# Performance work log

Hardware: AMD Instinct MI355X
Metric: run time of the kernel (lower is better)

The kernel has to match this reference:

```python
import jax, jax.numpy as jnp
import numpy as np

N, E = 50000, 800000
F_IN, F_OUT, H, F_EDGE = 256, 32, 8, 5
LEAKY_SLOPE = 0.2


def setup_inputs() -> dict:
    key = jax.random.key(0)
    ks = jax.random.split(key, 6)
    x = jax.random.normal(ks[0], (N, F_IN), dtype=jnp.float32)
    edge_index = jax.random.randint(ks[1], (2, E), 0, N, dtype=jnp.int64)
    edge_attr = jax.random.normal(ks[2], (E, F_EDGE), dtype=jnp.float32)
    degree_src = jax.random.randint(ks[3], (E,), 0, 64, dtype=jnp.int64)
    # Xavier-uniform params
    lim_W = float(np.sqrt(6.0 / (F_IN + F_OUT)))
    W = jax.random.uniform(ks[4], (H, F_IN, F_OUT), minval=-lim_W, maxval=lim_W, dtype=jnp.float32)
    A = 2 * F_OUT + F_EDGE
    lim_a = float(np.sqrt(6.0 / (H + A)))
    a = jax.random.uniform(ks[5], (H, A), minval=-lim_a, maxval=lim_a, dtype=jnp.float32)
    lim_e = float(np.sqrt(1.0 / F_EDGE))
    W_edge_w = jax.random.uniform(jax.random.fold_in(key, 7), (F_EDGE, F_EDGE), minval=-lim_e, maxval=lim_e, dtype=jnp.float32)
    return {"x": x, "edge_index": edge_index, "edge_attr": edge_attr,
            "degree_src": degree_src, "W": W, "a": a, "W_edge_w": W_edge_w}


def reference(x, edge_index, edge_attr, degree_src, W, a, W_edge_w):
    n = x.shape[0]
    h, f_out = W.shape[0], W.shape[2]
    src, dst = edge_index[0], edge_index[1]
    # per-head projection: (N, H, F_out)
    Wh = jnp.einsum('nf,hfo->nho', x, W)
    # split attention vector instead of materializing the concat
    a_src, a_dst, a_e = a[:, :f_out], a[:, f_out:2 * f_out], a[:, 2 * f_out:]
    ef = edge_attr @ W_edge_w.T                      # (E, F_edge)
    e = (jnp.einsum('eho,ho->eh', Wh[src], a_src)
         + jnp.einsum('eho,ho->eh', Wh[dst], a_dst)
         + ef @ a_e.T)                                # (E, H)
    e = jax.nn.leaky_relu(e, LEAKY_SLOPE)
    scale = 1.0 / jnp.sqrt(jnp.clip(degree_src.astype(jnp.float32), 1.0, None))
    e = e * scale[:, None]
    # segment softmax over src; torch scatter_reduce amax include_self=True with zeros init -> max includes 0
    e_max = jnp.maximum(jax.ops.segment_max(e, src, num_segments=n), 0.0)
    e_exp = jnp.exp(e - e_max[src])
    e_sum = jax.ops.segment_sum(e_exp, src, num_segments=n)
    alpha = e_exp / (e_sum[src] + 1e-16)             # (E, H)
    msg = Wh[dst] * alpha[:, :, None]                # (E, H, F_out)
    out = jax.ops.segment_sum(msg, src, num_segments=n)
    out = jax.nn.elu(out.reshape(n, h * f_out))
    return out, alpha
```

## Files before the change

kernel.cpp:

```cpp
#include <hip/hip_runtime.h>
#include <hip/hip_bf16.h>
#include <math.h>

#define NN 50000
#define NE 800000
#define FIN 256
#define FOUT 32
#define NH 8
#define FE 5
#define AROW 69
#define NROWS_PAD 50048
#define BSTRIDE 48
#define ASTRIDE 264

typedef float f32x4 __attribute__((ext_vector_type(4)));
typedef short bf16x8 __attribute__((ext_vector_type(8)));

static __device__ __forceinline__ unsigned short f2bf(float f) {
    unsigned u = __float_as_uint(f);
    unsigned r = (u + 0x7FFFu + ((u >> 16) & 1u)) >> 16;
    return (unsigned short)r;
}
static __device__ __forceinline__ float bf2f(unsigned short b) {
    return __uint_as_float(((unsigned)b) << 16);
}
static __device__ __forceinline__ short f2bf_fast(float f) {
    __hip_bfloat16 h = __float2bfloat16(f);
    return *reinterpret_cast<short*>(&h);
}

__global__ __launch_bounds__(256) void k_prepre(const float* __restrict__ W,
                                                const float* __restrict__ a,
                                                const float* __restrict__ Wew,
                                                const int* __restrict__ ei,
                                                float* __restrict__ C,
                                                unsigned short* __restrict__ Bh,
                                                unsigned short* __restrict__ Bsh,
                                                unsigned short* __restrict__ Bsl,
                                                int* __restrict__ counts,
                                                int* __restrict__ pos) {
    int b = blockIdx.x, t = threadIdx.x;
    int i = b * 256 + t;
    if (i < NE / 4) {
        int4 e4 = *(const int4*)&ei[i * 4];
        int4 pv;
        pv.x = atomicAdd(&counts[e4.x], 1);
        pv.y = atomicAdd(&counts[e4.y], 1);
        pv.z = atomicAdd(&counts[e4.z], 1);
        pv.w = atomicAdd(&counts[e4.w], 1);
        *(int4*)&pos[i * 4] = pv;
    }
    if (b < 256) {
        int c = b, k = t;
        int h = c >> 5, o = c & 31;
        Bh[c * 256 + k] = f2bf(W[(size_t)h * (FIN * FOUT) + (size_t)k * FOUT + o]);
    } else if (b == 256) {
        if (t < NH * FE) {
            int h = t / FE, k = t % FE;
            float s = 0.f;
            for (int j = 0; j < FE; ++j) s += a[h * AROW + 2 * FOUT + j] * Wew[j * FE + k];
            C[t] = s;
        }
        int k = t;
        for (int h = 0; h < NH; ++h) {
            float s1v = 0.f, s2v = 0.f;
            for (int o = 0; o < FOUT; ++o) {
                float wv = W[(size_t)h * (FIN * FOUT) + (size_t)k * FOUT + o];
                s1v += wv * a[h * AROW + o];
                s2v += wv * a[h * AROW + FOUT + o];
            }
            unsigned short h1 = f2bf(s1v);
            Bsh[h * 256 + k] = h1;
            Bsl[h * 256 + k] = f2bf(s1v - bf2f(h1));
            unsigned short h2 = f2bf(s2v);
            Bsh[(8 + h) * 256 + k] = h2;
            Bsl[(8 + h) * 256 + k] = f2bf(s2v - bf2f(h2));
        }
    }
}

__global__ __launch_bounds__(256) void k_gemm_mfma(const float* __restrict__ x,
                                                   const unsigned short* __restrict__ Bh,
                                                   const unsigned short* __restrict__ Bsh,
                                                   const unsigned short* __restrict__ Bsl,
                                                   unsigned short* __restrict__ Whb,
                                                   float* __restrict__ s1,
                                                   float* __restrict__ s2, int nrows) {
    __shared__ __align__(16) unsigned short Ah[64 * ASTRIDE];
    int t = threadIdx.x;
    int w = t >> 6, l = t & 63;
    int r = l & 15, blk = l >> 4;
    int row0 = blockIdx.x * 64;
    int c0 = w * 64;

#pragma unroll
    for (int i = 0; i < 16; ++i) {
        int row = row0 + w * 16 + i;
        if (row >= nrows) row = nrows - 1;
        f32x4 u = *(const f32x4*)&x[(size_t)row * 256 + l * 4];
        short b0 = f2bf_fast(u.x), b1 = f2bf_fast(u.y);
        short b2 = f2bf_fast(u.z), b3 = f2bf_fast(u.w);
        ushort4 pk;
        pk.x = (unsigned short)b0; pk.y = (unsigned short)b1;
        pk.z = (unsigned short)b2; pk.w = (unsigned short)b3;
        *(ushort4*)&Ah[(w * 16 + i) * ASTRIDE + l * 4] = pk;
    }
    __syncthreads();

    f32x4 acc[4][4];
    f32x4 acc_s = (f32x4)(0.f);
#pragma unroll
    for (int i = 0; i < 4; ++i)
#pragma unroll
        for (int j = 0; j < 4; ++j) acc[i][j] = (f32x4)(0.f);

    const unsigned short* bp0 = &Bh[(c0 + 0 * 16 + r) * 256 + blk * 8];
    const unsigned short* bp1 = &Bh[(c0 + 1 * 16 + r) * 256 + blk * 8];
    const unsigned short* bp2 = &Bh[(c0 + 2 * 16 + r) * 256 + blk * 8];
    const unsigned short* bp3 = &Bh[(c0 + 3 * 16 + r) * 256 + blk * 8];

#pragma unroll
    for (int ks = 0; ks < 8; ++ks) {
        const int k0 = ks * 32;
        bf16x8 ah[4];
#pragma unroll
        for (int rt = 0; rt < 4; ++rt)
            ah[rt] = *(const bf16x8*)&Ah[(rt * 16 + r) * ASTRIDE + k0 + blk * 8];
        bf16x8 bh[4];
        bh[0] = *(const bf16x8*)(bp0 + k0);
        bh[1] = *(const bf16x8*)(bp1 + k0);
        bh[2] = *(const bf16x8*)(bp2 + k0);
        bh[3] = *(const bf16x8*)(bp3 + k0);
#pragma unroll
        for (int ct = 0; ct < 4; ++ct) {
#pragma unroll
            for (int rt = 0; rt < 4; ++rt)
                acc[rt][ct] = __builtin_amdgcn_mfma_f32_16x16x32_bf16(ah[rt], bh[ct], acc[rt][ct], 0, 0, 0);
        }
        {
            bf16x8 bsh = *(const bf16x8*)&Bsh[r * 256 + k0 + blk * 8];
            bf16x8 bsl = *(const bf16x8*)&Bsl[r * 256 + k0 + blk * 8];
            acc_s = __builtin_amdgcn_mfma_f32_16x16x32_bf16(ah[w], bsh, acc_s, 0, 0, 0);
            acc_s = __builtin_amdgcn_mfma_f32_16x16x32_bf16(ah[w], bsl, acc_s, 0, 0, 0);
        }
    }

#pragma unroll
    for (int rt = 0; rt < 4; ++rt) {
#pragma unroll
        for (int reg = 0; reg < 4; ++reg) {
            int row = row0 + rt * 16 + blk * 4 + reg;
            if (row < nrows) {
#pragma unroll
                for (int ct = 0; ct < 4; ++ct)
                    Whb[(size_t)row * 256 + c0 + ct * 16 + r] = f2bf(acc[rt][ct][reg]);
            }
        }
    }
#pragma unroll
    for (int reg = 0; reg < 4; ++reg) {
        int row = row0 + w * 16 + blk * 4 + reg;
        if (row < nrows) {
            if (r < 8) s1[row * NH + r] = acc_s[reg];
            else       s2[row * NH + (r - 8)] = acc_s[reg];
        }
    }
}

__global__ __launch_bounds__(256) void k_scatlog(const int* __restrict__ ei,
                                                 const float* __restrict__ eattr,
                                                 const int* __restrict__ degs,
                                                 const float* __restrict__ s1,
                                                 const float* __restrict__ s2,
                                                 const float* __restrict__ C,
                                                 const int* __restrict__ pos,
                                                 unsigned short* __restrict__ e_perm,
                                                 int2* __restrict__ de_perm) {
    __shared__ float Cl[NH * FE];
    int t = threadIdx.x;
    if (t < NH * FE) Cl[t] = C[t];
    __syncthreads();
    int e = blockIdx.x * 256 + t;
    if (e >= NE) return;
    int src = ei[e], dst = ei[NE + e];
    int dg = degs[e];
    float scale = rsqrtf((float)(dg > 1 ? dg : 1));
    float ea0 = eattr[(size_t)e * FE + 0];
    float ea1 = eattr[(size_t)e * FE + 1];
    float ea2 = eattr[(size_t)e * FE + 2];
    float ea3 = eattr[(size_t)e * FE + 3];
    float ea4 = eattr[(size_t)e * FE + 4];
    float4 s1a = *(const float4*)&s1[src * NH];
    float4 s1b = *(const float4*)&s1[src * NH + 4];
    float4 s2a = *(const float4*)&s2[dst * NH];
    float4 s2b = *(const float4*)&s2[dst * NH + 4];
    float vs1[8] = {s1a.x, s1a.y, s1a.z, s1a.w, s1b.x, s1b.y, s1b.z, s1b.w};
    float vs2[8] = {s2a.x, s2a.y, s2a.z, s2a.w, s2b.x, s2b.y, s2b.z, s2b.w};
    bf16x8 v;
#pragma unroll
    for (int h = 0; h < NH; ++h) {
        float q = vs1[h] + vs2[h] + ea0 * Cl[h * FE + 0] + ea1 * Cl[h * FE + 1] +
                  ea2 * Cl[h * FE + 2] + ea3 * Cl[h * FE + 3] + ea4 * Cl[h * FE + 4];
        q = q > 0.f ? q : 0.2f * q;
        v[h] = (short)f2bf(q * scale);
    }
    int ps = pos[e];
    if (ps < BSTRIDE) {
        int p = src * BSTRIDE + ps;
        *(bf16x8*)&e_perm[(size_t)p * 8] = v;
        de_perm[p] = make_int2(dst, e);
    }
}

__global__ __launch_bounds__(256) void k_smmsg(const int* __restrict__ counts,
                                               const unsigned short* __restrict__ e_perm,
                                               const int2* __restrict__ de_perm,
                                               const unsigned short* __restrict__ Whb,
                                               float* __restrict__ out_alpha,
                                               float* __restrict__ out) {
    __shared__ float al[4][256];
    __shared__ int dl[4][32];
    __shared__ int el[4][32];
    int t = threadIdx.x;
    int w = t >> 6, l = t & 63;
    int n = blockIdx.x * 4 + w;
    if (n >= NN) return;
    int start = n * BSTRIDE;
    int deg = counts[n];
    if (deg > BSTRIDE) deg = BSTRIDE;
    int j = l >> 3, h = l & 7;

    float vc[4];
#pragma unroll
    for (int q = 0; q < 4; ++q) {
        int b = j + 8 * q;
        vc[q] = (b < deg) ? bf2f(e_perm[(size_t)(start + b) * 8 + h]) : -1e30f;
    }
    float mx = 0.f;
#pragma unroll
    for (int q = 0; q < 4; ++q) mx = fmaxf(mx, vc[q]);
    for (int b = 32 + j; b < deg; b += 8)
        mx = fmaxf(mx, bf2f(e_perm[(size_t)(start + b) * 8 + h]));
    mx = fmaxf(mx, __shfl_xor(mx, 8));
    mx = fmaxf(mx, __shfl_xor(mx, 16));
    mx = fmaxf(mx, __shfl_xor(mx, 32));
    float m = mx;
    float ex[4];
    float sm = 0.f;
#pragma unroll
    for (int q = 0; q < 4; ++q) { ex[q] = __expf(vc[q] - m); sm += ex[q]; }
    for (int b = 32 + j; b < deg; b += 8)
        sm += __expf(bf2f(e_perm[(size_t)(start + b) * 8 + h]) - m);
    sm += __shfl_xor(sm, 8);
    sm += __shfl_xor(sm, 16);
    sm += __shfl_xor(sm, 32);
    float inv = 1.f / (sm + 1e-16f);
    f32x4 acc = (f32x4)(0.f);
    int hh = l >> 3;
    for (int base = 0; base < deg; base += 32) {
        int cnt = deg - base;
        if (cnt > 32) cnt = 32;
        if (l < cnt) {
            int2 de = de_perm[start + base + l];
            dl[w][l] = de.x;
            el[w][l] = de.y;
        }
        asm volatile("s_waitcnt lgkmcnt(0)" ::: "memory");
#pragma unroll
        for (int q = 0; q < 4; ++q) {
            int b = base + j + 8 * q;
            if (b < deg) {
                float av = (base == 0 ? ex[q]
                                      : __expf(bf2f(e_perm[(size_t)(start + b) * 8 + h]) - m)) * inv;
                al[w][(j + 8 * q) * 8 + h] = av;
                out_alpha[(size_t)el[w][j + 8 * q] * 8 + h] = av;
            }
        }
        asm volatile("s_waitcnt lgkmcnt(0)" ::: "memory");
        int jj = 0;
        for (; jj + 4 <= cnt; jj += 4) {
            int d0 = dl[w][jj], d1 = dl[w][jj + 1], d2 = dl[w][jj + 2], d3 = dl[w][jj + 3];
            float a0 = al[w][jj * 8 + hh],      a1 = al[w][jj * 8 + 8 + hh];
            float a2 = al[w][jj * 8 + 16 + hh], a3 = al[w][jj * 8 + 24 + hh];
            ushort4 u0 = *(const ushort4*)&Whb[(size_t)d0 * 256 + l * 4];
            ushort4 u1 = *(const ushort4*)&Whb[(size_t)d1 * 256 + l * 4];
            ushort4 u2 = *(const ushort4*)&Whb[(size_t)d2 * 256 + l * 4];
            ushort4 u3 = *(const ushort4*)&Whb[(size_t)d3 * 256 + l * 4];
            acc.x += a0 * bf2f(u0.x) + a1 * bf2f(u1.x) + a2 * bf2f(u2.x) + a3 * bf2f(u3.x);
            acc.y += a0 * bf2f(u0.y) + a1 * bf2f(u1.y) + a2 * bf2f(u2.y) + a3 * bf2f(u3.y);
            acc.z += a0 * bf2f(u0.z) + a1 * bf2f(u1.z) + a2 * bf2f(u2.z) + a3 * bf2f(u3.z);
            acc.w += a0 * bf2f(u0.w) + a1 * bf2f(u1.w) + a2 * bf2f(u2.w) + a3 * bf2f(u3.w);
        }
        for (; jj < cnt; ++jj) {
            int d0 = dl[w][jj];
            float a0 = al[w][jj * 8 + hh];
            ushort4 u0 = *(const ushort4*)&Whb[(size_t)d0 * 256 + l * 4];
            acc.x += a0 * bf2f(u0.x);
            acc.y += a0 * bf2f(u0.y);
            acc.z += a0 * bf2f(u0.z);
            acc.w += a0 * bf2f(u0.w);
        }
        asm volatile("s_waitcnt lgkmcnt(0)" ::: "memory");
    }
    f32x4 o;
    o.x = acc.x > 0.f ? acc.x : expm1f(acc.x);
    o.y = acc.y > 0.f ? acc.y : expm1f(acc.y);
    o.z = acc.z > 0.f ? acc.z : expm1f(acc.z);
    o.w = acc.w > 0.f ? acc.w : expm1f(acc.w);
    *(f32x4*)&out[(size_t)n * 256 + l * 4] = o;
}

extern "C" void kernel_launch(void* const* d_in, const int* in_sizes, int n_in,
                              void* d_out, int out_size, void* d_ws, size_t ws_size,
                              hipStream_t stream) {
    const float* x     = (const float*)d_in[0];
    const int*   ei    = (const int*)d_in[1];
    const float* eattr = (const float*)d_in[2];
    const int*   degs  = (const int*)d_in[3];
    const float* W     = (const float*)d_in[4];
    const float* a     = (const float*)d_in[5];
    const float* Wew   = (const float*)d_in[6];

    float* out       = (float*)d_out;
    float* out_alpha = out + (size_t)NN * 256;

    char* p = (char*)d_ws;
    auto alloc = [&](size_t bytes) -> char* {
        char* r = p;
        p += (bytes + 255) & ~(size_t)255;
        return r;
    };
    unsigned short* Whb     = (unsigned short*)alloc((size_t)NN * 256 * 2);
    float*          s1      = (float*)alloc((size_t)NN * NH * 4);
    float*          s2      = (float*)alloc((size_t)NN * NH * 4);
    float*          Cm      = (float*)alloc(NH * FE * 4);
    unsigned short* Bh      = (unsigned short*)alloc((size_t)256 * 256 * 2);
    unsigned short* Bsh     = (unsigned short*)alloc((size_t)16 * 256 * 2);
    unsigned short* Bsl     = (unsigned short*)alloc((size_t)16 * 256 * 2);
    int*            counts  = (int*)alloc((size_t)NN * 4);
    int*            pos     = (int*)alloc((size_t)NE * 4);
    unsigned short* e_perm  = (unsigned short*)alloc(((size_t)NN * BSTRIDE + 64) * NH * 2);
    int2*           de_perm = (int2*)alloc(((size_t)NN * BSTRIDE + 64) * 8);

    hipMemsetAsync(counts, 0, (size_t)NN * 4, stream);

    k_prepre<<<(NE / 4 + 255) / 256, 256, 0, stream>>>(W, a, Wew, ei, Cm, Bh,
                                                       Bsh, Bsl, counts, pos);
    k_gemm_mfma<<<NROWS_PAD / 64, 256, 0, stream>>>(x, Bh, Bsh, Bsl, Whb, s1, s2, NN);
    k_scatlog<<<(NE + 255) / 256, 256, 0, stream>>>(ei, eattr, degs, s1, s2, Cm,
                                                    pos, e_perm, de_perm);
    k_smmsg<<<(NN + 3) / 4, 256, 0, stream>>>(counts, e_perm, de_perm, Whb,
                                              out_alpha, out);
}
```

Before: 223.7 us.

## Pre-convert x to bf16 in prep kernel and stage GEMM output through LDS

The fp32-to-bf16 conversion of x moves into the first prep kernel, which writes a bf16 copy to workspace. The GEMM then reads A fragments directly from global memory instead of staging them in shared memory. GEMM results are written into an LDS tile and stored as coalesced 8-byte row writes instead of scattered 2-byte stores. This adds an extra full write and read of a 25MB bf16 buffer, and the padded rows 50000-50047 of xb are never initialised, so the GEMM reads uninitialised memory for those rows.

```diff
diff --git a/kernel.cpp b/kernel.cpp
--- a/kernel.cpp
+++ b/kernel.cpp
@@ -11,7 +11,7 @@
 #define AROW 69
 #define NROWS_PAD 50048
 #define BSTRIDE 48
-#define ASTRIDE 264
+#define CSTRIDE 264
 
 typedef float f32x4 __attribute__((ext_vector_type(4)));
 typedef short bf16x8 __attribute__((ext_vector_type(8)));
@@ -32,15 +32,27 @@
 __global__ __launch_bounds__(256) void k_prepre(const float* __restrict__ W,
                                                 const float* __restrict__ a,
                                                 const float* __restrict__ Wew,
+                                                const float* __restrict__ x,
                                                 const int* __restrict__ ei,
                                                 float* __restrict__ C,
                                                 unsigned short* __restrict__ Bh,
                                                 unsigned short* __restrict__ Bsh,
                                                 unsigned short* __restrict__ Bsl,
+                                                unsigned short* __restrict__ xb,
                                                 int* __restrict__ counts,
                                                 int* __restrict__ pos) {
     int b = blockIdx.x, t = threadIdx.x;
     int i = b * 256 + t;
+    if (i < (NN * FIN) / 8) {
+        f32x4 u0 = *(const f32x4*)&x[(size_t)i * 8];
+        f32x4 u1 = *(const f32x4*)&x[(size_t)i * 8 + 4];
+        bf16x8 hi;
+        hi[0] = f2bf_fast(u0.x); hi[1] = f2bf_fast(u0.y);
+        hi[2] = f2bf_fast(u0.z); hi[3] = f2bf_fast(u0.w);
+        hi[4] = f2bf_fast(u1.x); hi[5] = f2bf_fast(u1.y);
+        hi[6] = f2bf_fast(u1.z); hi[7] = f2bf_fast(u1.w);
+        *(bf16x8*)&xb[(size_t)i * 8] = hi;
+    }
     if (i < NE / 4) {
         int4 e4 = *(const int4*)&ei[i * 4];
         int4 pv;
@@ -79,34 +91,20 @@
     }
 }
 
-__global__ __launch_bounds__(256) void k_gemm_mfma(const float* __restrict__ x,
+__global__ __launch_bounds__(256) void k_gemm_mfma(const unsigned short* __restrict__ xb,
                                                    const unsigned short* __restrict__ Bh,
                                                    const unsigned short* __restrict__ Bsh,
                                                    const unsigned short* __restrict__ Bsl,
                                                    unsigned short* __restrict__ Whb,
                                                    float* __restrict__ s1,
                                                    float* __restrict__ s2, int nrows) {
-    __shared__ __align__(16) unsigned short Ah[64 * ASTRIDE];
+    __shared__ __align__(16) unsigned short Ct[64 * CSTRIDE];
     int t = threadIdx.x;
     int w = t >> 6, l = t & 63;
     int r = l & 15, blk = l >> 4;
     int row0 = blockIdx.x * 64;
     int c0 = w * 64;
 
-#pragma unroll
-    for (int i = 0; i < 16; ++i) {
-        int row = row0 + w * 16 + i;
-        if (row >= nrows) row = nrows - 1;
-        f32x4 u = *(const f32x4*)&x[(size_t)row * 256 + l * 4];
-        short b0 = f2bf_fast(u.x), b1 = f2bf_fast(u.y);
-        short b2 = f2bf_fast(u.z), b3 = f2bf_fast(u.w);
-        ushort4 pk;
-        pk.x = (unsigned short)b0; pk.y = (unsigned short)b1;
-        pk.z = (unsigned short)b2; pk.w = (unsigned short)b3;
-        *(ushort4*)&Ah[(w * 16 + i) * ASTRIDE + l * 4] = pk;
-    }
-    __syncthreads();
-
     f32x4 acc[4][4];
     f32x4 acc_s = (f32x4)(0.f);
 #pragma unroll
@@ -114,10 +112,10 @@
 #pragma unroll
         for (int j = 0; j < 4; ++j) acc[i][j] = (f32x4)(0.f);
 
-    const unsigned short* bp0 = &Bh[(c0 + 0 * 16 + r) * 256 + blk * 8];
-    const unsigned short* bp1 = &Bh[(c0 + 1 * 16 + r) * 256 + blk * 8];
-    const unsigned short* bp2 = &Bh[(c0 + 2 * 16 + r) * 256 + blk * 8];
-    const unsigned short* bp3 = &Bh[(c0 + 3 * 16 + r) * 256 + blk * 8];
+    const unsigned short* ap[4];
+#pragma unroll
+    for (int rt = 0; rt < 4; ++rt)
+        ap[rt] = xb + (size_t)(row0 + rt * 16 + r) * 256 + blk * 8;
 
 #pragma unroll
     for (int ks = 0; ks < 8; ++ks) {
@@ -125,12 +123,13 @@
         bf16x8 ah[4];
 #pragma unroll
         for (int rt = 0; rt < 4; ++rt)
-            ah[rt] = *(const bf16x8*)&Ah[(rt * 16 + r) * ASTRIDE + k0 + blk * 8];
+            ah[rt] = *(const bf16x8*)(ap[rt] + k0);
         bf16x8 bh[4];
-        bh[0] = *(const bf16x8*)(bp0 + k0);
-        bh[1] = *(const bf16x8*)(bp1 + k0);
-        bh[2] = *(const bf16x8*)(bp2 + k0);
-        bh[3] = *(const bf16x8*)(bp3 + k0);
+#pragma unroll
+        for (int ct = 0; ct < 4; ++ct) {
+            int c = c0 + ct * 16 + r;
+            bh[ct] = *(const bf16x8*)&Bh[c * 256 + k0 + blk * 8];
+        }
 #pragma unroll
         for (int ct = 0; ct < 4; ++ct) {
 #pragma unroll
@@ -146,15 +145,20 @@
     }
 
 #pragma unroll
-    for (int rt = 0; rt < 4; ++rt) {
-#pragma unroll
-        for (int reg = 0; reg < 4; ++reg) {
-            int row = row0 + rt * 16 + blk * 4 + reg;
-            if (row < nrows) {
-#pragma unroll
-                for (int ct = 0; ct < 4; ++ct)
-                    Whb[(size_t)row * 256 + c0 + ct * 16 + r] = f2bf(acc[rt][ct][reg]);
-            }
+    for (int rt = 0; rt < 4; ++rt)
+#pragma unroll
+        for (int reg = 0; reg < 4; ++reg)
+#pragma unroll
+            for (int ct = 0; ct < 4; ++ct)
+                Ct[(rt * 16 + blk * 4 + reg) * CSTRIDE + c0 + ct * 16 + r] =
+                    f2bf(acc[rt][ct][reg]);
+    __syncthreads();
+#pragma unroll
+    for (int i = 0; i < 16; ++i) {
+        int row = row0 + w * 16 + i;
+        if (row < nrows) {
+            ushort4 v = *(const ushort4*)&Ct[(w * 16 + i) * CSTRIDE + l * 4];
+            *(ushort4*)&Whb[(size_t)row * 256 + l * 4] = v;
         }
     }
 #pragma unroll
@@ -331,6 +335,7 @@
         return r;
     };
     unsigned short* Whb     = (unsigned short*)alloc((size_t)NN * 256 * 2);
+    unsigned short* xb      = (unsigned short*)alloc((size_t)NROWS_PAD * 256 * 2);
     float*          s1      = (float*)alloc((size_t)NN * NH * 4);
     float*          s2      = (float*)alloc((size_t)NN * NH * 4);
     float*          Cm      = (float*)alloc(NH * FE * 4);
@@ -344,9 +349,9 @@
 
     hipMemsetAsync(counts, 0, (size_t)NN * 4, stream);
 
-    k_prepre<<<(NE / 4 + 255) / 256, 256, 0, stream>>>(W, a, Wew, ei, Cm, Bh,
-                                                       Bsh, Bsl, counts, pos);
-    k_gemm_mfma<<<NROWS_PAD / 64, 256, 0, stream>>>(x, Bh, Bsh, Bsl, Whb, s1, s2, NN);
+    k_prepre<<<(NN * FIN / 8 + 255) / 256, 256, 0, stream>>>(W, a, Wew, x, ei, Cm, Bh,
+                                                             Bsh, Bsl, xb, counts, pos);
+    k_gemm_mfma<<<NROWS_PAD / 64, 256, 0, stream>>>(xb, Bh, Bsh, Bsl, Whb, s1, s2, NN);
     k_scatlog<<<(NE + 255) / 256, 256, 0, stream>>>(ei, eattr, degs, s1, s2, Cm,
                                                     pos, e_perm, de_perm);
     k_smmsg<<<(NN + 3) / 4, 256, 0, stream>>>(counts, e_perm, de_perm, Whb,
```

After: 230.1 us. 1.03x slower.
